# Kernel optimization log

Hardware: AMD Instinct MI355X
Metric: run time of the kernel (lower is better)

The kernel has to match this reference:

```python
import jax, jax.numpy as jnp
import numpy as np

B, S, L, F, CD, NH, E, HID = 4, 1024, 256, 512, 768, 8, 8, 2048


def _xavier(k, shape):
    std = float(np.sqrt(1.0 / (shape[-2] + shape[-1])))
    return jax.random.normal(k, shape, dtype=jnp.float32) * std


def setup_inputs() -> dict:
    key = jax.random.key(0)
    ks = iter(jax.random.split(key, 64))
    nk = lambda: next(ks)
    inp = {}
    inp['x_r'] = jax.random.normal(nk(), (B, S, F), jnp.float32)
    inp['x_i'] = jax.random.normal(nk(), (B, S, F), jnp.float32)
    inp['ctx_r'] = jax.random.normal(nk(), (B, L, CD), jnp.float32)
    inp['ctx_i'] = jax.random.normal(nk(), (B, L, CD), jnp.float32)
    inp['ln1_g'] = jnp.ones((F,), jnp.float32)
    inp['ln2_g'] = jnp.ones((F,), jnp.float32)
    inp['ln3_g'] = jnp.ones((F,), jnp.float32)
    for pref, shp in [('sa_q', (F, F)), ('sa_k', (F, F)), ('sa_v', (F, F)), ('sa_o', (F, F)),
                      ('ca_q', (F, F)), ('ca_k', (CD, F)), ('ca_v', (CD, F)), ('ca_o', (F, F))]:
        inp[pref + 'Wr'] = _xavier(nk(), shp)
        inp[pref + 'Wi'] = _xavier(nk(), shp)
        inp[pref + 'br'] = jnp.zeros((F,), jnp.float32)
        inp[pref + 'bi'] = jnp.zeros((F,), jnp.float32)
    inp['moe_W1r'] = _xavier(nk(), (E, F, HID))
    inp['moe_W1i'] = _xavier(nk(), (E, F, HID))
    inp['moe_b1r'] = jnp.zeros((E, HID), jnp.float32)
    inp['moe_b1i'] = jnp.zeros((E, HID), jnp.float32)
    inp['moe_mb'] = jnp.zeros((E, HID), jnp.float32)  # modReLU bias
    inp['moe_W2r'] = _xavier(nk(), (E, HID, F))
    inp['moe_W2i'] = _xavier(nk(), (E, HID, F))
    inp['moe_b2r'] = jnp.zeros((E, F), jnp.float32)
    inp['moe_b2i'] = jnp.zeros((E, F), jnp.float32)
    return inp


def _clin(xr, xi, Wr, Wi, br, bi):
    # (xr + i xi) @ (Wr + i Wi) + (br + i bi)
    return xr @ Wr - xi @ Wi + br, xr @ Wi + xi @ Wr + bi


def _cln(xr, xi, g, eps=1e-6):
    amp = jnp.sqrt(xr * xr + xi * xi + eps)
    s = g * (amp / (jnp.mean(amp, axis=-1, keepdims=True) + eps)) / (amp + eps)
    return xr * s, xi * s


def _modrelu(xr, xi, b, eps=1e-10):
    amp = jnp.sqrt(xr * xr + xi * xi + eps)
    s = jax.nn.relu(amp + b) / (amp + eps)
    return xr * s, xi * s


def _cattn(xr, xi, cr, ci, qWr, qWi, qbr, qbi, kWr, kWi, kbr, kbi,
           vWr, vWi, vbr, vbi, oWr, oWi, obr, obi, nh):
    qr, qi = _clin(xr, xi, qWr, qWi, qbr, qbi)
    kr, ki = _clin(cr, ci, kWr, kWi, kbr, kbi)
    vr, vi = _clin(cr, ci, vWr, vWi, vbr, vbi)
    Bt, Sq, Ft = qr.shape
    Sk = kr.shape[1]
    d = Ft // nh
    sp = lambda t: t.reshape(Bt, t.shape[1], nh, d).transpose(0, 2, 1, 3)  # b n s d
    Qr, Qi, Kr, Ki, Vr, Vi = sp(qr), sp(qi), sp(kr), sp(ki), sp(vr), sp(vi)
    scale = 1.0 / float(d) ** 0.5
    scores = (jnp.einsum('bnqd,bnkd->bnqk', Qr, Kr)
              + jnp.einsum('bnqd,bnkd->bnqk', Qi, Ki)) * scale
    w = jax.nn.softmax(scores, axis=-1)
    mix = lambda t: jnp.einsum('bnqk,bnkd->bnqd', w, t).transpose(0, 2, 1, 3).reshape(Bt, Sq, Ft)
    return _clin(mix(Vr), mix(Vi), oWr, oWi, obr, obi)


def reference(x_r, x_i, ctx_r, ctx_i, ln1_g, ln2_g, ln3_g,
              sa_qWr, sa_qWi, sa_qbr, sa_qbi, sa_kWr, sa_kWi, sa_kbr, sa_kbi,
              sa_vWr, sa_vWi, sa_vbr, sa_vbi, sa_oWr, sa_oWi, sa_obr, sa_obi,
              ca_qWr, ca_qWi, ca_qbr, ca_qbi, ca_kWr, ca_kWi, ca_kbr, ca_kbi,
              ca_vWr, ca_vWi, ca_vbr, ca_vbi, ca_oWr, ca_oWi, ca_obr, ca_obi,
              moe_W1r, moe_W1i, moe_b1r, moe_b1i, moe_mb,
              moe_W2r, moe_W2i, moe_b2r, moe_b2i):
    # self-attention block
    hr, hi = _cln(x_r, x_i, ln1_g)
    ar, ai = _cattn(hr, hi, hr, hi, sa_qWr, sa_qWi, sa_qbr, sa_qbi,
                    sa_kWr, sa_kWi, sa_kbr, sa_kbi, sa_vWr, sa_vWi, sa_vbr, sa_vbi,
                    sa_oWr, sa_oWi, sa_obr, sa_obi, NH)
    xr, xi = x_r + ar, x_i + ai
    # cross-attention block
    hr, hi = _cln(xr, xi, ln2_g)
    ar, ai = _cattn(hr, hi, ctx_r, ctx_i, ca_qWr, ca_qWi, ca_qbr, ca_qbi,
                    ca_kWr, ca_kWi, ca_kbr, ca_kbi, ca_vWr, ca_vWi, ca_vbr, ca_vbi,
                    ca_oWr, ca_oWi, ca_obr, ca_obi, NH)
    xr, xi = xr + ar, xi + ai
    # phase-routed MoE block
    hr, hi = _cln(xr, xi, ln3_g)
    phase = jnp.arctan2(hi, hr)
    token_phase = jnp.arctan2(jnp.mean(jnp.sin(phase), axis=-1),
                              jnp.mean(jnp.cos(phase), axis=-1))
    idx = jnp.clip(jnp.floor((token_phase + jnp.pi) / (2.0 * jnp.pi) * E).astype(jnp.int32), 0, E - 1)
    acc_r = jnp.zeros_like(hr)
    acc_i = jnp.zeros_like(hi)
    for e in range(E):  # dense-compute-then-mask, faithful to source
        ur, ui = _clin(hr, hi, moe_W1r[e], moe_W1i[e], moe_b1r[e], moe_b1i[e])
        ur, ui = _modrelu(ur, ui, moe_mb[e])
        yr, yi = _clin(ur, ui, moe_W2r[e], moe_W2i[e], moe_b2r[e], moe_b2i[e])
        m = (idx == e).astype(hr.dtype)[..., None]
        acc_r = acc_r + yr * m
        acc_i = acc_i + yi * m
    xr, xi = xr + acc_r, xi + acc_i
    return jnp.stack([xr, xi])  # [2, B, S, F] real/imag
```

## Files before the change

kernel.cpp:

```cpp
#include <hip/hip_runtime.h>
#include <hip/hip_bf16.h>
#include <math.h>


#define NTOK 4096
#define FF   512
#define CDIM 768
#define NEXP 8
#define HID  2048
#define TMAX 72
#define NPAD (TMAX * 64)

typedef __hip_bfloat16 bf16;
typedef short bf16x8 __attribute__((ext_vector_type(8)));
typedef float f32x4  __attribute__((ext_vector_type(4)));

__device__ __forceinline__ short f2bf(float x) {
    unsigned u = __float_as_uint(x);
    unsigned r = (u + 0x7fff + ((u >> 16) & 1)) >> 16;
    return (short)r;
}
__device__ __forceinline__ float bf2f(short s) {
    return __uint_as_float(((unsigned)(unsigned short)s) << 16);
}

__global__ __launch_bounds__(256)
void cln_kernel(const float* __restrict__ xr, const float* __restrict__ xi,
                const float* __restrict__ g,
                float* __restrict__ hr, float* __restrict__ hi)
{
    const int F = FF;
    long base = (long)blockIdx.x * F;
    int t = threadIdx.x;
    int j0 = t, j1 = t + 256;
    float xr0 = xr[base + j0], xi0 = xi[base + j0];
    float xr1 = xr[base + j1], xi1 = xi[base + j1];
    float a0 = sqrtf(xr0 * xr0 + xi0 * xi0 + 1e-6f);
    float a1 = sqrtf(xr1 * xr1 + xi1 * xi1 + 1e-6f);
    float s = a0 + a1;
#pragma unroll
    for (int off = 32; off >= 1; off >>= 1) s += __shfl_xor(s, off);
    __shared__ float wsum[4];
    if ((t & 63) == 0) wsum[t >> 6] = s;
    __syncthreads();
    float mean = (wsum[0] + wsum[1] + wsum[2] + wsum[3]) * (1.0f / 512.0f);
    float d0 = g[j0] * (a0 / (mean + 1e-6f)) / (a0 + 1e-6f);
    float d1 = g[j1] * (a1 / (mean + 1e-6f)) / (a1 + 1e-6f);
    hr[base + j0] = xr0 * d0;  hi[base + j0] = xi0 * d0;
    hr[base + j1] = xr1 * d1;  hi[base + j1] = xi1 * d1;
}

__global__ __launch_bounds__(256)
void expandA_x3(const float* __restrict__ sR, const float* __restrict__ sI,
                bf16* __restrict__ dR, bf16* __restrict__ dI, int K)
{
    int k = blockIdx.x * 256 + threadIdx.x;
    int m = blockIdx.y;
    long s = (long)m * K + k;
    long d = (long)m * 3 * K + k;
    float a = sR[s];
    bf16 ah = __float2bfloat16(a);
    bf16 al = __float2bfloat16(a - __bfloat162float(ah));
    dR[d] = ah; dR[d + K] = al; dR[d + 2 * K] = ah;
    float b = sI[s];
    bf16 bh = __float2bfloat16(b);
    bf16 bl = __float2bfloat16(b - __bfloat162float(bh));
    dI[d] = bh; dI[d + K] = bl; dI[d + 2 * K] = bh;
}

__global__ __launch_bounds__(256)
void convA_plain(const float* __restrict__ sR, const float* __restrict__ sI,
                 bf16* __restrict__ dR, bf16* __restrict__ dI, int K)
{
    int k = blockIdx.x * 256 + threadIdx.x;
    long s = (long)blockIdx.y * K + k;
    dR[s] = __float2bfloat16(sR[s]);
    dI[s] = __float2bfloat16(sI[s]);
}

__global__ __launch_bounds__(256)
void expandW_x3_packed(const float* __restrict__ sR, const float* __restrict__ sI,
                       bf16* __restrict__ dR, bf16* __restrict__ dI,
                       int N, int kdiv )
{
    int g = blockIdx.x * 256 + threadIdx.x;
    int nt = g >> 6, l = g & 63;
    int kc = blockIdx.y;
    int t3 = (kc >= kdiv) + (kc >= 2 * kdiv);
    int kb = (kc - t3 * kdiv) * 32 + (l >> 4) * 8;
    int n  = nt * 16 + (l & 15);
    long dbase = ((long)kc * (N >> 4) + nt) * 512 + l * 8;
#pragma unroll
    for (int j = 0; j < 8; j++) {
        float a = sR[(long)(kb + j) * N + n];
        bf16 ah = __float2bfloat16(a);
        dR[dbase + j] = (t3 < 2) ? ah : __float2bfloat16(a - __bfloat162float(ah));
        float b = sI[(long)(kb + j) * N + n];
        bf16 bh = __float2bfloat16(b);
        dI[dbase + j] = (t3 < 2) ? bh : __float2bfloat16(b - __bfloat162float(bh));
    }
}

__global__ __launch_bounds__(256)
void convW_packed(const float* __restrict__ sR, const float* __restrict__ sI,
                  bf16* __restrict__ dR, bf16* __restrict__ dI,
                  int N, long estride)
{
    int g = blockIdx.x * 256 + threadIdx.x;
    int nt = g >> 6, l = g & 63;
    int kc = blockIdx.y;
    int e  = blockIdx.z;
    const float* srcR = sR + (long)e * estride;
    const float* srcI = sI + (long)e * estride;
    bf16* dstR = dR + (long)e * estride;
    bf16* dstI = dI + (long)e * estride;
    int kb = kc * 32 + (l >> 4) * 8;
    int n  = nt * 16 + (l & 15);
    long dbase = ((long)kc * (N >> 4) + nt) * 512 + l * 8;
#pragma unroll
    for (int j = 0; j < 8; j++) {
        dstR[dbase + j] = __float2bfloat16(srcR[(long)(kb + j) * N + n]);
        dstI[dbase + j] = __float2bfloat16(srcI[(long)(kb + j) * N + n]);
    }
}

template<bool EXPERT, bool GATHER, bool MODRELU, bool RESID, bool OUTBF16>
__global__ __launch_bounds__(256)
void cgemm_mfma(const bf16* __restrict__ Ar, const bf16* __restrict__ Ai, int lda,
                const bf16* __restrict__ Wr, const bf16* __restrict__ Wi,
                long wstride, int ntTot,
                const float* __restrict__ br, const float* __restrict__ bi, int bstride,
                const float* __restrict__ mb,
                const float* __restrict__ Rr, const float* __restrict__ Ri,
                void* __restrict__ Crv, void* __restrict__ Civ, int ldc, int Kp,
                const int* __restrict__ order, const int* __restrict__ tileExpert)
{
    __shared__ short sA[8192];
    __shared__ short sW[8192];
    int tm = blockIdx.x, tn = blockIdx.y;
    if (EXPERT) {
        int e = tileExpert[tm];
        if (e < 0) return;
        Wr += (long)e * wstride;  Wi += (long)e * wstride;
        br += (long)e * bstride;  bi += (long)e * bstride;
        if (MODRELU) mb += (long)e * bstride;
    }
    int t = threadIdx.x;
    int m = t & 63, jj = t >> 6;
    int aldsLane = (jj << 4) + (m & 15);
    int mt = m >> 4;
    long abase; bool aok = true;
    {
        int arow = tm * 64 + m;
        if (GATHER) { int g = order[arow]; aok = (g >= 0); abase = (long)(aok ? g : 0) * lda; }
        else abase = (long)arow * lda;
    }
    int wl = t & 63, wb = t >> 6;
    int l = t & 63, w = t >> 6;
    int wm = w & 1, wn = w >> 1;

    f32x4 z = {0.f, 0.f, 0.f, 0.f};
    f32x4 accR[2][2], accI[2][2];
#pragma unroll
    for (int a = 0; a < 2; a++)
#pragma unroll
        for (int b = 0; b < 2; b++) { accR[a][b] = z; accI[a][b] = z; }

    const bf16x8 sgn = {(short)0x8000,(short)0x8000,(short)0x8000,(short)0x8000,
                        (short)0x8000,(short)0x8000,(short)0x8000,(short)0x8000};

    for (int k0 = 0; k0 < Kp; k0 += 64) {
        __syncthreads();
#pragma unroll
        for (int ri = 0; ri < 2; ri++) {
            const bf16* src = ri ? Ai : Ar;
#pragma unroll
            for (int kc = 0; kc < 2; kc++) {
                bf16x8 v = {};
                if (!GATHER || aok)
                    v = *(const bf16x8*)&src[abase + k0 + kc * 32 + jj * 8];
                *(bf16x8*)&sA[((((ri * 2 + kc) << 2) + mt) << 9) + aldsLane * 8] = v;
            }
        }
        int kc0 = k0 >> 5;
#pragma unroll
        for (int it = 0; it < 4; it++) {
            int b  = (it << 2) + wb;
            int ri = b >> 3, kc = (b >> 2) & 1, ntl = b & 3;
            const bf16* src = ri ? Wi : Wr;
            bf16x8 v = *(const bf16x8*)&src[(((long)(kc0 + kc) * ntTot + tn * 4 + ntl) << 9) + wl * 8];
            *(bf16x8*)&sW[((((ri * 2 + kc) << 2) + ntl) << 9) + wl * 8] = v;
        }
        __syncthreads();
#pragma unroll
        for (int kc = 0; kc < 2; kc++) {
            bf16x8 arf[2], aif[2], naf[2], wrf[2], wif[2];
#pragma unroll
            for (int s = 0; s < 2; s++) {
                arf[s] = *(const bf16x8*)&sA[(((kc << 2) + wm * 2 + s) << 9) + l * 8];
                aif[s] = *(const bf16x8*)&sA[((((2 + kc) << 2) + wm * 2 + s) << 9) + l * 8];
                naf[s] = aif[s] ^ sgn;
                wrf[s] = *(const bf16x8*)&sW[(((kc << 2) + wn * 2 + s) << 9) + l * 8];
                wif[s] = *(const bf16x8*)&sW[((((2 + kc) << 2) + wn * 2 + s) << 9) + l * 8];
            }
#pragma unroll
            for (int sm = 0; sm < 2; sm++)
#pragma unroll
                for (int sn = 0; sn < 2; sn++) {
                    accR[sm][sn] = __builtin_amdgcn_mfma_f32_16x16x32_bf16(arf[sm], wrf[sn], accR[sm][sn], 0, 0, 0);
                    accR[sm][sn] = __builtin_amdgcn_mfma_f32_16x16x32_bf16(naf[sm], wif[sn], accR[sm][sn], 0, 0, 0);
                    accI[sm][sn] = __builtin_amdgcn_mfma_f32_16x16x32_bf16(arf[sm], wif[sn], accI[sm][sn], 0, 0, 0);
                    accI[sm][sn] = __builtin_amdgcn_mfma_f32_16x16x32_bf16(aif[sm], wrf[sn], accI[sm][sn], 0, 0, 0);
                }
        }
    }
#pragma unroll
    for (int sm = 0; sm < 2; sm++)
#pragma unroll
        for (int sn = 0; sn < 2; sn++) {
            int row0 = tm * 64 + (wm * 2 + sm) * 16 + (l >> 4) * 4;
            int col  = tn * 64 + (wn * 2 + sn) * 16 + (l & 15);
            float bre = br[col], bie = bi[col];
            float mbe = MODRELU ? mb[col] : 0.f;
#pragma unroll
            for (int v = 0; v < 4; v++) {
                int row = row0 + v;
                float vr = accR[sm][sn][v] + bre;
                float vi = accI[sm][sn][v] + bie;
                if (MODRELU) {
                    float amp = sqrtf(vr * vr + vi * vi + 1e-10f);
                    float sc = fmaxf(amp + mbe, 0.f) / (amp + 1e-10f);
                    vr *= sc; vi *= sc;
                }
                long cidx = (long)row * ldc + col;
                if (RESID) { vr += Rr[cidx]; vi += Ri[cidx]; }
                if (OUTBF16) {
                    ((bf16*)Crv)[cidx] = __float2bfloat16(vr);
                    ((bf16*)Civ)[cidx] = __float2bfloat16(vi);
                } else {
                    ((float*)Crv)[cidx] = vr;
                    ((float*)Civ)[cidx] = vi;
                }
            }
        }
}

__global__ __launch_bounds__(256)
void cattn_mfma(const float* __restrict__ qr, const float* __restrict__ qi,
                const float* __restrict__ kr, const float* __restrict__ ki,
                const float* __restrict__ vr, const float* __restrict__ vi,
                float* __restrict__ mr, float* __restrict__ mi,
                int S, int Sk)
{
    __shared__ short sK[8192];
    __shared__ short sV[8192];
    __shared__ short sP[5120];
    const int F = FF;
    int qt = blockIdx.x, h = blockIdx.y, b = blockIdx.z;
    int t = threadIdx.x;
    int w = t >> 6, l = t & 63, q = l >> 4, n16 = l & 15;

    bf16x8 qh_[2][2], ql_[2][2];
    {
        long qbase = ((long)(b * S + qt * 64 + w * 16 + n16)) * F + h * 64 + q * 8;
#pragma unroll
        for (int ri = 0; ri < 2; ri++) {
            const float* src = ri ? qi : qr;
#pragma unroll
            for (int c = 0; c < 2; c++) {
#pragma unroll
                for (int j = 0; j < 8; j++) {
                    float x = src[qbase + c * 32 + j];
                    short xh = f2bf(x);
                    qh_[ri][c][j] = xh;
                    ql_[ri][c][j] = f2bf(x - bf2f(xh));
                }
            }
        }
    }

    f32x4 zf = {0.f, 0.f, 0.f, 0.f};
    f32x4 oR[4], oI[4];
#pragma unroll
    for (int nt = 0; nt < 4; nt++) { oR[nt] = zf; oI[nt] = zf; }
    float m_run[4] = {-3.0e38f, -3.0e38f, -3.0e38f, -3.0e38f};
    float l_run[4] = {0.f, 0.f, 0.f, 0.f};

    int nkt = Sk >> 5;
    for (int kt = 0; kt < nkt; kt++) {
        __syncthreads();
#pragma unroll
        for (int it = 0; it < 2; it++) {
            int s = t + 256 * it;
            int sl = s & 63, g = s >> 6;
            int ri = g >> 2, c = (g >> 1) & 1, nt = g & 1;
            int sq = sl >> 4, sn = sl & 15;
            const float* src = ri ? ki : kr;
            long base = ((long)(b * Sk + kt * 32 + nt * 16 + sn)) * F + h * 64 + c * 32 + sq * 8;
            int outH = ((((ri * 2 + 0) * 2 + c) * 2 + nt) * 64 + sl) * 8;
            int outL = ((((ri * 2 + 1) * 2 + c) * 2 + nt) * 64 + sl) * 8;
#pragma unroll
            for (int j = 0; j < 8; j++) {
                float x = src[base + j];
                short xh = f2bf(x);
                sK[outH + j] = xh;
                sK[outL + j] = f2bf(x - bf2f(xh));
            }
        }
#pragma unroll
        for (int it = 0; it < 2; it++) {
            int s = t + 256 * it;
            int sl = s & 63, g = s >> 6;
            int ri = g >> 2, nt = g & 3;
            int sq = sl >> 4, sn = sl & 15;
            const float* src = ri ? vi : vr;
            long base = ((long)(b * Sk + kt * 32 + sq * 8)) * F + h * 64 + nt * 16 + sn;
            int outH = (((ri * 2 + 0) * 4 + nt) * 64 + sl) * 8;
            int outL = (((ri * 2 + 1) * 4 + nt) * 64 + sl) * 8;
#pragma unroll
            for (int j = 0; j < 8; j++) {
                float x = src[base + (long)j * F];
                short xh = f2bf(x);
                sV[outH + j] = xh;
                sV[outL + j] = f2bf(x - bf2f(xh));
            }
        }
        __syncthreads();

        f32x4 sc[2];
        sc[0] = zf; sc[1] = zf;
#pragma unroll
        for (int nt = 0; nt < 2; nt++) {
#pragma unroll
            for (int ri = 0; ri < 2; ri++) {
                bf16x8 kh0 = *(const bf16x8*)&sK[((((ri * 2 + 0) * 2 + 0) * 2 + nt) * 64 + l) * 8];
                bf16x8 kh1 = *(const bf16x8*)&sK[((((ri * 2 + 0) * 2 + 1) * 2 + nt) * 64 + l) * 8];
                bf16x8 kl0 = *(const bf16x8*)&sK[((((ri * 2 + 1) * 2 + 0) * 2 + nt) * 64 + l) * 8];
                bf16x8 kl1 = *(const bf16x8*)&sK[((((ri * 2 + 1) * 2 + 1) * 2 + nt) * 64 + l) * 8];
                sc[nt] = __builtin_amdgcn_mfma_f32_16x16x32_bf16(qh_[ri][0], kh0, sc[nt], 0, 0, 0);
                sc[nt] = __builtin_amdgcn_mfma_f32_16x16x32_bf16(qh_[ri][1], kh1, sc[nt], 0, 0, 0);
                sc[nt] = __builtin_amdgcn_mfma_f32_16x16x32_bf16(ql_[ri][0], kh0, sc[nt], 0, 0, 0);
                sc[nt] = __builtin_amdgcn_mfma_f32_16x16x32_bf16(ql_[ri][1], kh1, sc[nt], 0, 0, 0);
                sc[nt] = __builtin_amdgcn_mfma_f32_16x16x32_bf16(qh_[ri][0], kl0, sc[nt], 0, 0, 0);
                sc[nt] = __builtin_amdgcn_mfma_f32_16x16x32_bf16(qh_[ri][1], kl1, sc[nt], 0, 0, 0);
            }
        }
        float alpha[4];
#pragma unroll
        for (int v = 0; v < 4; v++) {
            float s0 = sc[0][v] * 0.125f, s1 = sc[1][v] * 0.125f;
            float mx = fmaxf(s0, s1);
            mx = fmaxf(mx, __shfl_xor(mx, 1));
            mx = fmaxf(mx, __shfl_xor(mx, 2));
            mx = fmaxf(mx, __shfl_xor(mx, 4));
            mx = fmaxf(mx, __shfl_xor(mx, 8));
            float mnew = fmaxf(m_run[v], mx);
            float p0 = expf(s0 - mnew), p1 = expf(s1 - mnew);
            sc[0][v] = p0; sc[1][v] = p1;
            float ps = p0 + p1;
            ps += __shfl_xor(ps, 1);
            ps += __shfl_xor(ps, 2);
            ps += __shfl_xor(ps, 4);
            ps += __shfl_xor(ps, 8);
            alpha[v] = expf(m_run[v] - mnew);
            l_run[v] = l_run[v] * alpha[v] + ps;
            m_run[v] = mnew;
        }
#pragma unroll
        for (int nt = 0; nt < 4; nt++)
#pragma unroll
            for (int v = 0; v < 4; v++) { oR[nt][v] *= alpha[v]; oI[nt][v] *= alpha[v]; }
        int pbase = w * 1280;
#pragma unroll
        for (int nt = 0; nt < 2; nt++)
#pragma unroll
            for (int v = 0; v < 4; v++) {
                float p = sc[nt][v];
                short ph = f2bf(p);
                short pl = f2bf(p - bf2f(ph));
                int idx = pbase + (q * 4 + v) * 40 + nt * 16 + n16;
                sP[idx] = ph;
                sP[idx + 640] = pl;
            }
        bf16x8 pH = *(const bf16x8*)&sP[pbase + n16 * 40 + q * 8];
        bf16x8 pL = *(const bf16x8*)&sP[pbase + 640 + n16 * 40 + q * 8];
#pragma unroll
        for (int nt = 0; nt < 4; nt++) {
            bf16x8 vh = *(const bf16x8*)&sV[(((0 * 2 + 0) * 4 + nt) * 64 + l) * 8];
            bf16x8 vl = *(const bf16x8*)&sV[(((0 * 2 + 1) * 4 + nt) * 64 + l) * 8];
            oR[nt] = __builtin_amdgcn_mfma_f32_16x16x32_bf16(pH, vh, oR[nt], 0, 0, 0);
            oR[nt] = __builtin_amdgcn_mfma_f32_16x16x32_bf16(pL, vh, oR[nt], 0, 0, 0);
            oR[nt] = __builtin_amdgcn_mfma_f32_16x16x32_bf16(pH, vl, oR[nt], 0, 0, 0);
            bf16x8 wh = *(const bf16x8*)&sV[(((1 * 2 + 0) * 4 + nt) * 64 + l) * 8];
            bf16x8 wl2 = *(const bf16x8*)&sV[(((1 * 2 + 1) * 4 + nt) * 64 + l) * 8];
            oI[nt] = __builtin_amdgcn_mfma_f32_16x16x32_bf16(pH, wh, oI[nt], 0, 0, 0);
            oI[nt] = __builtin_amdgcn_mfma_f32_16x16x32_bf16(pL, wh, oI[nt], 0, 0, 0);
            oI[nt] = __builtin_amdgcn_mfma_f32_16x16x32_bf16(pH, wl2, oI[nt], 0, 0, 0);
        }
    }
#pragma unroll
    for (int v = 0; v < 4; v++) {
        float inv = 1.0f / l_run[v];
        long obase = ((long)(b * S + qt * 64 + w * 16 + q * 4 + v)) * F + h * 64 + n16;
#pragma unroll
        for (int nt = 0; nt < 4; nt++) {
            mr[obase + nt * 16] = oR[nt][v] * inv;
            mi[obase + nt * 16] = oI[nt][v] * inv;
        }
    }
}

__global__ __launch_bounds__(256)
void route_kernel(const float* __restrict__ hr, const float* __restrict__ hi,
                  int* __restrict__ eidx)
{
    const int F = FF;
    long base = (long)blockIdx.x * F;
// ... 87 lines not shown
extern "C" void kernel_launch(void* const* d_in, const int* in_sizes, int n_in,
                              void* d_out, int out_size, void* d_ws, size_t ws_size,
                              hipStream_t stream)
{
    (void)in_sizes; (void)n_in; (void)out_size; (void)ws_size;
    const float* x_r   = (const float*)d_in[0];
    const float* x_i   = (const float*)d_in[1];
    const float* ctx_r = (const float*)d_in[2];
    const float* ctx_i = (const float*)d_in[3];
    const float* ln1_g = (const float*)d_in[4];
    const float* ln2_g = (const float*)d_in[5];
    const float* ln3_g = (const float*)d_in[6];
    const float* sa_qWr = (const float*)d_in[7];   const float* sa_qWi = (const float*)d_in[8];
    const float* sa_qbr = (const float*)d_in[9];   const float* sa_qbi = (const float*)d_in[10];
    const float* sa_kWr = (const float*)d_in[11];  const float* sa_kWi = (const float*)d_in[12];
    const float* sa_kbr = (const float*)d_in[13];  const float* sa_kbi = (const float*)d_in[14];
    const float* sa_vWr = (const float*)d_in[15];  const float* sa_vWi = (const float*)d_in[16];
    const float* sa_vbr = (const float*)d_in[17];  const float* sa_vbi = (const float*)d_in[18];
    const float* sa_oWr = (const float*)d_in[19];  const float* sa_oWi = (const float*)d_in[20];
    const float* sa_obr = (const float*)d_in[21];  const float* sa_obi = (const float*)d_in[22];
    const float* ca_qWr = (const float*)d_in[23];  const float* ca_qWi = (const float*)d_in[24];
    const float* ca_qbr = (const float*)d_in[25];  const float* ca_qbi = (const float*)d_in[26];
    const float* ca_kWr = (const float*)d_in[27];  const float* ca_kWi = (const float*)d_in[28];
    const float* ca_kbr = (const float*)d_in[29];  const float* ca_kbi = (const float*)d_in[30];
    const float* ca_vWr = (const float*)d_in[31];  const float* ca_vWi = (const float*)d_in[32];
    const float* ca_vbr = (const float*)d_in[33];  const float* ca_vbi = (const float*)d_in[34];
    const float* ca_oWr = (const float*)d_in[35];  const float* ca_oWi = (const float*)d_in[36];
    const float* ca_obr = (const float*)d_in[37];  const float* ca_obi = (const float*)d_in[38];
    const float* moe_W1r = (const float*)d_in[39]; const float* moe_W1i = (const float*)d_in[40];
    const float* moe_b1r = (const float*)d_in[41]; const float* moe_b1i = (const float*)d_in[42];
    const float* moe_mb  = (const float*)d_in[43];
    const float* moe_W2r = (const float*)d_in[44]; const float* moe_W2i = (const float*)d_in[45];
    const float* moe_b2r = (const float*)d_in[46]; const float* moe_b2i = (const float*)d_in[47];
    float* out = (float*)d_out;

    char* W = (char*)d_ws;
    const long NF = (long)NTOK * FF;
    float* xr = (float*)(W + 0 * NF * 4);
    float* xi = (float*)(W + 1 * NF * 4);
    float* hr = (float*)(W + 2 * NF * 4);
    float* hi = (float*)(W + 3 * NF * 4);
    char* poolB = W + 4 * NF * 4;
    float* qr = (float*)poolB;                float* qi = (float*)(poolB + NF * 4);
    float* kr = (float*)(poolB + 2 * NF * 4); float* ki = (float*)(poolB + 3 * NF * 4);
    float* vr = (float*)(poolB + 4 * NF * 4); float* vi = (float*)(poolB + 5 * NF * 4);
    float* mr = (float*)(poolB + 6 * NF * 4); float* mi = (float*)(poolB + 7 * NF * 4);
    bf16* u_r = (bf16*)poolB;
    bf16* u_i = (bf16*)(poolB + 18874368);
    float* y_r = (float*)(poolB + 37748736);
    float* y_i = (float*)(poolB + 37748736 + 9437184);
    bf16* h3r = (bf16*)(poolB + 56623104);
    bf16* h3i = (bf16*)(poolB + 56623104 + 4194304);
    char* Q = W + 12 * NF * 4;
    bf16* A1r = (bf16*)Q;                   bf16* A1i = (bf16*)(Q + 12582912);
    bf16* A2r = (bf16*)(Q + 25165824);      bf16* A2i = (bf16*)(Q + 25165824 + 4718592);
    char* WQ = Q + 34603008;
    bf16* saq_r = (bf16*)(WQ + 0 * 1572864);  bf16* saq_i = (bf16*)(WQ + 1 * 1572864);
    bf16* sak_r = (bf16*)(WQ + 2 * 1572864);  bf16* sak_i = (bf16*)(WQ + 3 * 1572864);
    bf16* sav_r = (bf16*)(WQ + 4 * 1572864);  bf16* sav_i = (bf16*)(WQ + 5 * 1572864);
    bf16* sao_r = (bf16*)(WQ + 6 * 1572864);  bf16* sao_i = (bf16*)(WQ + 7 * 1572864);
    bf16* caq_r = (bf16*)(WQ + 8 * 1572864);  bf16* caq_i = (bf16*)(WQ + 9 * 1572864);
    bf16* cao_r = (bf16*)(WQ + 10 * 1572864); bf16* cao_i = (bf16*)(WQ + 11 * 1572864);
    bf16* cak_r = (bf16*)(WQ + 12 * 1572864);
    bf16* cak_i = (bf16*)(WQ + 12 * 1572864 + 2359296);
    bf16* cav_r = (bf16*)(WQ + 12 * 1572864 + 2 * 2359296);
    bf16* cav_i = (bf16*)(WQ + 12 * 1572864 + 3 * 2359296);
    bf16* Wm_r = (bf16*)Q;
    bf16* Wm_i = (bf16*)(Q + 16777216);
    int* eidx       = (int*)(W + 12 * NF * 4 + 62914560);
    int* order      = eidx + NTOK;
    int* tileExpert = order + NPAD;

    dim3 blk(256);
    const long W1S = (long)FF * HID;

    expandW_x3_packed<<<dim3(8, 48), blk, 0, stream>>>(sa_qWr, sa_qWi, saq_r, saq_i, FF, 16);
    expandW_x3_packed<<<dim3(8, 48), blk, 0, stream>>>(sa_kWr, sa_kWi, sak_r, sak_i, FF, 16);
    expandW_x3_packed<<<dim3(8, 48), blk, 0, stream>>>(sa_vWr, sa_vWi, sav_r, sav_i, FF, 16);
    expandW_x3_packed<<<dim3(8, 48), blk, 0, stream>>>(sa_oWr, sa_oWi, sao_r, sao_i, FF, 16);
    expandW_x3_packed<<<dim3(8, 48), blk, 0, stream>>>(ca_qWr, ca_qWi, caq_r, caq_i, FF, 16);
    expandW_x3_packed<<<dim3(8, 48), blk, 0, stream>>>(ca_oWr, ca_oWi, cao_r, cao_i, FF, 16);
    expandW_x3_packed<<<dim3(8, 72), blk, 0, stream>>>(ca_kWr, ca_kWi, cak_r, cak_i, FF, 24);
    expandW_x3_packed<<<dim3(8, 72), blk, 0, stream>>>(ca_vWr, ca_vWi, cav_r, cav_i, FF, 24);

    cln_kernel<<<NTOK, blk, 0, stream>>>(x_r, x_i, ln1_g, hr, hi);
    expandA_x3<<<dim3(2, NTOK), blk, 0, stream>>>(hr, hi, A1r, A1i, FF);
    cgemm_mfma<false,false,false,false,false><<<dim3(64, 8), blk, 0, stream>>>(
        A1r, A1i, 1536, saq_r, saq_i, 0, 32, sa_qbr, sa_qbi, 0, nullptr,
        nullptr, nullptr, qr, qi, FF, 1536, nullptr, nullptr);
    cgemm_mfma<false,false,false,false,false><<<dim3(64, 8), blk, 0, stream>>>(
        A1r, A1i, 1536, sak_r, sak_i, 0, 32, sa_kbr, sa_kbi, 0, nullptr,
        nullptr, nullptr, kr, ki, FF, 1536, nullptr, nullptr);
    cgemm_mfma<false,false,false,false,false><<<dim3(64, 8), blk, 0, stream>>>(
        A1r, A1i, 1536, sav_r, sav_i, 0, 32, sa_vbr, sa_vbi, 0, nullptr,
        nullptr, nullptr, vr, vi, FF, 1536, nullptr, nullptr);
    cattn_mfma<<<dim3(16, 8, 4), blk, 0, stream>>>(qr, qi, kr, ki, vr, vi,
                                                   mr, mi, 1024, 1024);
    expandA_x3<<<dim3(2, NTOK), blk, 0, stream>>>(mr, mi, A1r, A1i, FF);
    cgemm_mfma<false,false,false,true,false><<<dim3(64, 8), blk, 0, stream>>>(
        A1r, A1i, 1536, sao_r, sao_i, 0, 32, sa_obr, sa_obi, 0, nullptr,
        x_r, x_i, xr, xi, FF, 1536, nullptr, nullptr);

    cln_kernel<<<NTOK, blk, 0, stream>>>(xr, xi, ln2_g, hr, hi);
    expandA_x3<<<dim3(2, NTOK), blk, 0, stream>>>(hr, hi, A1r, A1i, FF);
    cgemm_mfma<false,false,false,false,false><<<dim3(64, 8), blk, 0, stream>>>(
        A1r, A1i, 1536, caq_r, caq_i, 0, 32, ca_qbr, ca_qbi, 0, nullptr,
        nullptr, nullptr, qr, qi, FF, 1536, nullptr, nullptr);
    expandA_x3<<<dim3(3, 1024), blk, 0, stream>>>(ctx_r, ctx_i, A2r, A2i, CDIM);
    cgemm_mfma<false,false,false,false,false><<<dim3(16, 8), blk, 0, stream>>>(
        A2r, A2i, 2304, cak_r, cak_i, 0, 32, ca_kbr, ca_kbi, 0, nullptr,
        nullptr, nullptr, kr, ki, FF, 2304, nullptr, nullptr);
    cgemm_mfma<false,false,false,false,false><<<dim3(16, 8), blk, 0, stream>>>(
        A2r, A2i, 2304, cav_r, cav_i, 0, 32, ca_vbr, ca_vbi, 0, nullptr,
        nullptr, nullptr, vr, vi, FF, 2304, nullptr, nullptr);
    cattn_mfma<<<dim3(16, 8, 4), blk, 0, stream>>>(qr, qi, kr, ki, vr, vi,
                                                   mr, mi, 1024, 256);
    expandA_x3<<<dim3(2, NTOK), blk, 0, stream>>>(mr, mi, A1r, A1i, FF);
    cgemm_mfma<false,false,false,true,false><<<dim3(64, 8), blk, 0, stream>>>(
        A1r, A1i, 1536, cao_r, cao_i, 0, 32, ca_obr, ca_obi, 0, nullptr,
        xr, xi, xr, xi, FF, 1536, nullptr, nullptr);

    cln_kernel<<<NTOK, blk, 0, stream>>>(xr, xi, ln3_g, hr, hi);
    route_kernel<<<NTOK, blk, 0, stream>>>(hr, hi, eidx);
    moe_build_kernel<<<1, blk, 0, stream>>>(eidx, order, tileExpert);
    convA_plain<<<dim3(2, NTOK), blk, 0, stream>>>(hr, hi, h3r, h3i, FF);
    convW_packed<<<dim3(32, 16, 8), blk, 0, stream>>>(moe_W1r, moe_W1i, Wm_r, Wm_i, HID, W1S);
    cgemm_mfma<true,true,true,false,true><<<dim3(TMAX, 32), blk, 0, stream>>>(
        h3r, h3i, FF, Wm_r, Wm_i, W1S, 128, moe_b1r, moe_b1i, HID, moe_mb,
        nullptr, nullptr, u_r, u_i, HID, FF, order, tileExpert);
    convW_packed<<<dim3(8, 64, 8), blk, 0, stream>>>(moe_W2r, moe_W2i, Wm_r, Wm_i, FF, W1S);
    cgemm_mfma<true,false,false,false,false><<<dim3(TMAX, 8), blk, 0, stream>>>(
        u_r, u_i, HID, Wm_r, Wm_i, W1S, 32, moe_b2r, moe_b2i, FF, nullptr,
        nullptr, nullptr, y_r, y_i, FF, HID, order, tileExpert);
    combine_kernel<<<NPAD, blk, 0, stream>>>(order, xr, xi, y_r, y_i, out);
}
```

Measured before the change: 1.031 ms.

## Use async global-to-LDS loads, x2 split storage, batched QKV GEMMs, prepacked KV

The expanded bf16 split operands are now stored as only hi/lo (x2) instead of hi/lo/hi, and the GEMM remaps its K index on the fly so the third term reuses the hi part. This cuts expansion traffic and buffer size. GEMM tile loads use global_load_lds direct-to-LDS copies, and Q/K/V (plus cross-attn K/V) projections are batched into one launch via a z grid dimension. K/V are pre-split into packed bf16 hi/lo tiles by a separate kernel so attention can bulk-copy them, and expf becomes __expf. This adds a pack kernel, reuses buffers for the packed data, and the fast exp slightly changes numerics.

Result: faster. 894.5 us (-13.2%).

```diff
diff --git a/kernel.cpp b/kernel.cpp
--- a/kernel.cpp
+++ b/kernel.cpp
@@ -15,6 +15,8 @@
 typedef short bf16x8 __attribute__((ext_vector_type(8)));
 typedef float f32x4  __attribute__((ext_vector_type(4)));
 
+struct Ptr6 { const float* p[6]; };
+
 __device__ __forceinline__ short f2bf(float x) {
     unsigned u = __float_as_uint(x);
     unsigned r = (u + 0x7fff + ((u >> 16) & 1)) >> 16;
@@ -22,6 +24,11 @@
 }
 __device__ __forceinline__ float bf2f(short s) {
     return __uint_as_float(((unsigned)(unsigned short)s) << 16);
+}
+__device__ __forceinline__ void gload16(const void* g, void* l) {
+    __builtin_amdgcn_global_load_lds(
+        (const __attribute__((address_space(1))) unsigned int*)g,
+        (__attribute__((address_space(3))) unsigned int*)l, 16, 0, 0);
 }
 
 __global__ __launch_bounds__(256)
@@ -51,21 +58,19 @@
 }
 
 __global__ __launch_bounds__(256)
-void expandA_x3(const float* __restrict__ sR, const float* __restrict__ sI,
+void expandA_x2(const float* __restrict__ sR, const float* __restrict__ sI,
                 bf16* __restrict__ dR, bf16* __restrict__ dI, int K)
 {
     int k = blockIdx.x * 256 + threadIdx.x;
     int m = blockIdx.y;
     long s = (long)m * K + k;
-    long d = (long)m * 3 * K + k;
+    long d = (long)m * 2 * K + k;
     float a = sR[s];
     bf16 ah = __float2bfloat16(a);
-    bf16 al = __float2bfloat16(a - __bfloat162float(ah));
-    dR[d] = ah; dR[d + K] = al; dR[d + 2 * K] = ah;
+    dR[d] = ah; dR[d + K] = __float2bfloat16(a - __bfloat162float(ah));
     float b = sI[s];
     bf16 bh = __float2bfloat16(b);
-    bf16 bl = __float2bfloat16(b - __bfloat162float(bh));
-    dI[d] = bh; dI[d + K] = bl; dI[d + 2 * K] = bh;
+    dI[d] = bh; dI[d + K] = __float2bfloat16(b - __bfloat162float(bh));
 }
 
 __global__ __launch_bounds__(256)
@@ -79,25 +84,25 @@
 }
 
 __global__ __launch_bounds__(256)
-void expandW_x3_packed(const float* __restrict__ sR, const float* __restrict__ sI,
+void expandW_x2_packed(const float* __restrict__ sR, const float* __restrict__ sI,
                        bf16* __restrict__ dR, bf16* __restrict__ dI,
-                       int N, int kdiv )
+                       int N, int kdiv)
 {
     int g = blockIdx.x * 256 + threadIdx.x;
     int nt = g >> 6, l = g & 63;
     int kc = blockIdx.y;
-    int t3 = (kc >= kdiv) + (kc >= 2 * kdiv);
-    int kb = (kc - t3 * kdiv) * 32 + (l >> 4) * 8;
+    int lo = (kc >= kdiv);
+    int kb = (kc - (lo ? kdiv : 0)) * 32 + (l >> 4) * 8;
     int n  = nt * 16 + (l & 15);
     long dbase = ((long)kc * (N >> 4) + nt) * 512 + l * 8;
 #pragma unroll
     for (int j = 0; j < 8; j++) {
         float a = sR[(long)(kb + j) * N + n];
         bf16 ah = __float2bfloat16(a);
-        dR[dbase + j] = (t3 < 2) ? ah : __float2bfloat16(a - __bfloat162float(ah));
+        dR[dbase + j] = lo ? __float2bfloat16(a - __bfloat162float(ah)) : ah;
         float b = sI[(long)(kb + j) * N + n];
         bf16 bh = __float2bfloat16(b);
-        dI[dbase + j] = (t3 < 2) ? bh : __float2bfloat16(b - __bfloat162float(bh));
+        dI[dbase + j] = lo ? __float2bfloat16(b - __bfloat162float(bh)) : bh;
     }
 }
 
@@ -124,73 +129,75 @@
     }
 }
 
-template<bool EXPERT, bool GATHER, bool MODRELU, bool RESID, bool OUTBF16>
-__global__ __launch_bounds__(256)
-void cgemm_mfma(const bf16* __restrict__ Ar, const bf16* __restrict__ Ai, int lda,
-                const bf16* __restrict__ Wr, const bf16* __restrict__ Wi,
-                long wstride, int ntTot,
-                const float* __restrict__ br, const float* __restrict__ bi, int bstride,
-                const float* __restrict__ mb,
+template<bool X3, bool EXPERT, bool GATHER, bool MODRELU, bool RESID, bool OUTBF16>
+__global__ __launch_bounds__(256)
+void cgemm_mfma(const bf16* __restrict__ Ar, const bf16* __restrict__ Ai,
+                int lda, int Kreal,
+                const bf16* __restrict__ Wr0, const bf16* __restrict__ Wi0,
+                long wz, long westride, int ntTot, int kdiv,
+                Ptr6 bias, int bstride, const float* __restrict__ mb,
                 const float* __restrict__ Rr, const float* __restrict__ Ri,
-                void* __restrict__ Crv, void* __restrict__ Civ, int ldc, int Kp,
+                void* __restrict__ Cr0, void* __restrict__ Ci0, long cz,
+                int ldc, int Kp,
                 const int* __restrict__ order, const int* __restrict__ tileExpert)
 {
     __shared__ short sA[8192];
     __shared__ short sW[8192];
-    int tm = blockIdx.x, tn = blockIdx.y;
+    int tm = blockIdx.x, tn = blockIdx.y, z = blockIdx.z;
+    const bf16* Wr = Wr0 + (long)z * wz;
+    const bf16* Wi = Wi0 + (long)z * wz;
+    const float* br = bias.p[2 * z];
+    const float* bi = bias.p[2 * z + 1];
+    void* Crv = (char*)Cr0 + (long)z * cz;
+    void* Civ = (char*)Ci0 + (long)z * cz;
     if (EXPERT) {
         int e = tileExpert[tm];
         if (e < 0) return;
-        Wr += (long)e * wstride;  Wi += (long)e * wstride;
-        br += (long)e * bstride;  bi += (long)e * bstride;
+        Wr += (long)e * westride;  Wi += (long)e * westride;
+        br += (long)e * bstride;   bi += (long)e * bstride;
         if (MODRELU) mb += (long)e * bstride;
     }
     int t = threadIdx.x;
-    int m = t & 63, jj = t >> 6;
-    int aldsLane = (jj << 4) + (m & 15);
-    int mt = m >> 4;
-    long abase; bool aok = true;
-    {
-        int arow = tm * 64 + m;
-        if (GATHER) { int g = order[arow]; aok = (g >= 0); abase = (long)(aok ? g : 0) * lda; }
-        else abase = (long)arow * lda;
-    }
-    int wl = t & 63, wb = t >> 6;
-    int l = t & 63, w = t >> 6;
-    int wm = w & 1, wn = w >> 1;
-
-    f32x4 z = {0.f, 0.f, 0.f, 0.f};
+    int l = t & 63, jj = t >> 6;
+    int riS = jj >> 1, kcS = jj & 1;
+    const bf16* Asrc = riS ? Ai : Ar;
+    const bf16* Wsrc = riS ? Wi : Wr;
+    int kq8 = (l >> 4) * 8;
+    long arb[4];
+#pragma unroll
+    for (int mt = 0; mt < 4; mt++) {
+        int grow = tm * 64 + mt * 16 + (l & 15);
+        int tok = grow;
+        if (GATHER) { int gg = order[grow]; tok = (gg < 0) ? 0 : gg; }
+        arb[mt] = (long)tok * lda;
+    }
+    int wm = jj & 1, wn = jj >> 1;
+
+    f32x4 zf = {0.f, 0.f, 0.f, 0.f};
     f32x4 accR[2][2], accI[2][2];
 #pragma unroll
     for (int a = 0; a < 2; a++)
 #pragma unroll
-        for (int b = 0; b < 2; b++) { accR[a][b] = z; accI[a][b] = z; }
+        for (int b = 0; b < 2; b++) { accR[a][b] = zf; accI[a][b] = zf; }
 
     const bf16x8 sgn = {(short)0x8000,(short)0x8000,(short)0x8000,(short)0x8000,
                         (short)0x8000,(short)0x8000,(short)0x8000,(short)0x8000};
 
     for (int k0 = 0; k0 < Kp; k0 += 64) {
         __syncthreads();
-#pragma unroll
-        for (int ri = 0; ri < 2; ri++) {
-            const bf16* src = ri ? Ai : Ar;
-#pragma unroll
-            for (int kc = 0; kc < 2; kc++) {
-                bf16x8 v = {};
-                if (!GATHER || aok)
-                    v = *(const bf16x8*)&src[abase + k0 + kc * 32 + jj * 8];
-                *(bf16x8*)&sA[((((ri * 2 + kc) << 2) + mt) << 9) + aldsLane * 8] = v;
-            }
-        }
-        int kc0 = k0 >> 5;
-#pragma unroll
-        for (int it = 0; it < 4; it++) {
-            int b  = (it << 2) + wb;
-            int ri = b >> 3, kc = (b >> 2) & 1, ntl = b & 3;
-            const bf16* src = ri ? Wi : Wr;
-            bf16x8 v = *(const bf16x8*)&src[(((long)(kc0 + kc) * ntTot + tn * 4 + ntl) << 9) + wl * 8];
-            *(bf16x8*)&sW[((((ri * 2 + kc) << 2) + ntl) << 9) + wl * 8] = v;
-        }
+        int lc = k0 + kcS * 32;
+        int acol = (X3 && lc >= 2 * Kreal) ? lc - 2 * Kreal : lc;
+#pragma unroll
+        for (int mt = 0; mt < 4; mt++)
+            gload16(Asrc + arb[mt] + acol + kq8,
+                    &sA[(((riS * 2 + kcS) << 2) + mt) << 9]);
+        int kcl = (k0 >> 5) + kcS;
+        int pkc = (X3 && kcl >= kdiv) ? kcl - kdiv : kcl;
+        const bf16* wbase = Wsrc + (((long)pkc * ntTot + tn * 4) << 9) + l * 8;
+#pragma unroll
+        for (int ntl = 0; ntl < 4; ntl++)
+            gload16(wbase + (ntl << 9),
+                    &sW[(((riS * 2 + kcS) << 2) + ntl) << 9]);
         __syncthreads();
 #pragma unroll
         for (int kc = 0; kc < 2; kc++) {
@@ -246,9 +253,56 @@
 }
 
 __global__ __launch_bounds__(256)
+void pack_kv(const float* __restrict__ kr, const float* __restrict__ ki,
+             const float* __restrict__ vr, const float* __restrict__ vi,
+             short* __restrict__ pK, short* __restrict__ pV, int Sk)
+{
+    const int F = FF;
+    int kt = blockIdx.x, h = blockIdx.y, b = blockIdx.z;
+    int nkt = gridDim.x;
+    long blkbase = ((long)((b * 8 + h) * nkt) + kt) * 8192;
+    int t = threadIdx.x;
+#pragma unroll
+    for (int it = 0; it < 2; it++) {
+        int s = t + 256 * it;
+        int sl = s & 63, g = s >> 6;
+        int ri = g >> 2, c = (g >> 1) & 1, nt = g & 1;
+        int sq = sl >> 4, sn = sl & 15;
+        const float* src = ri ? ki : kr;
+        long base = ((long)(b * Sk + kt * 32 + nt * 16 + sn)) * F + h * 64 + c * 32 + sq * 8;
+        long outH = blkbase + ((((ri * 2 + 0) * 2 + c) * 2 + nt) * 64 + sl) * 8;
+        long outL = blkbase + ((((ri * 2 + 1) * 2 + c) * 2 + nt) * 64 + sl) * 8;
+#pragma unroll
+        for (int j = 0; j < 8; j++) {
+            float x = src[base + j];
+            short xh = f2bf(x);
+            pK[outH + j] = xh;
+            pK[outL + j] = f2bf(x - bf2f(xh));
+        }
+    }
+#pragma unroll
+    for (int it = 0; it < 2; it++) {
+        int s = t + 256 * it;
+        int sl = s & 63, g = s >> 6;
+        int ri = g >> 2, nt = g & 3;
+        int sq = sl >> 4, sn = sl & 15;
+        const float* src = ri ? vi : vr;
+        long base = ((long)(b * Sk + kt * 32 + sq * 8)) * F + h * 64 + nt * 16 + sn;
+        long outH = blkbase + (((ri * 2 + 0) * 4 + nt) * 64 + sl) * 8;
+        long outL = blkbase + (((ri * 2 + 1) * 4 + nt) * 64 + sl) * 8;
+#pragma unroll
+        for (int j = 0; j < 8; j++) {
+            float x = src[base + (long)j * F];
+            short xh = f2bf(x);
+            pV[outH + j] = xh;
+            pV[outL + j] = f2bf(x - bf2f(xh));
+        }
+    }
+}
+
+__global__ __launch_bounds__(256)
 void cattn_mfma(const float* __restrict__ qr, const float* __restrict__ qi,
-                const float* __restrict__ kr, const float* __restrict__ ki,
-                const float* __restrict__ vr, const float* __restrict__ vi,
+                const short* __restrict__ pK, const short* __restrict__ pV,
                 float* __restrict__ mr, float* __restrict__ mi,
                 int S, int Sk)
 {
@@ -268,12 +322,14 @@
             const float* src = ri ? qi : qr;
 #pragma unroll
             for (int c = 0; c < 2; c++) {
+                float vv[8];
+                *(float4*)&vv[0] = *(const float4*)&src[qbase + c * 32];
+                *(float4*)&vv[4] = *(const float4*)&src[qbase + c * 32 + 4];
 #pragma unroll
                 for (int j = 0; j < 8; j++) {
-                    float x = src[qbase + c * 32 + j];
-                    short xh = f2bf(x);
+                    short xh = f2bf(vv[j]);
                     qh_[ri][c][j] = xh;
-                    ql_[ri][c][j] = f2bf(x - bf2f(xh));
+                    ql_[ri][c][j] = f2bf(vv[j] - bf2f(xh));
                 }
             }
         }
@@ -287,43 +343,15 @@
     float l_run[4] = {0.f, 0.f, 0.f, 0.f};
 
     int nkt = Sk >> 5;
+    long pbh = (long)((b * 8 + h) * nkt) * 8192;
     for (int kt = 0; kt < nkt; kt++) {
         __syncthreads();
-#pragma unroll
-        for (int it = 0; it < 2; it++) {
-            int s = t + 256 * it;
-            int sl = s & 63, g = s >> 6;
-            int ri = g >> 2, c = (g >> 1) & 1, nt = g & 1;
-            int sq = sl >> 4, sn = sl & 15;
-            const float* src = ri ? ki : kr;
-            long base = ((long)(b * Sk + kt * 32 + nt * 16 + sn)) * F + h * 64 + c * 32 + sq * 8;
-            int outH = ((((ri * 2 + 0) * 2 + c) * 2 + nt) * 64 + sl) * 8;
-            int outL = ((((ri * 2 + 1) * 2 + c) * 2 + nt) * 64 + sl) * 8;
-#pragma unroll
-            for (int j = 0; j < 8; j++) {
-                float x = src[base + j];
-                short xh = f2bf(x);
-                sK[outH + j] = xh;
-                sK[outL + j] = f2bf(x - bf2f(xh));
-            }
-        }
-#pragma unroll
-        for (int it = 0; it < 2; it++) {
-            int s = t + 256 * it;
-            int sl = s & 63, g = s >> 6;
-            int ri = g >> 2, nt = g & 3;
-            int sq = sl >> 4, sn = sl & 15;
-            const float* src = ri ? vi : vr;
-            long base = ((long)(b * Sk + kt * 32 + sq * 8)) * F + h * 64 + nt * 16 + sn;
-            int outH = (((ri * 2 + 0) * 4 + nt) * 64 + sl) * 8;
-            int outL = (((ri * 2 + 1) * 4 + nt) * 64 + sl) * 8;
-#pragma unroll
-            for (int j = 0; j < 8; j++) {
-                float x = src[base + (long)j * F];
-                short xh = f2bf(x);
-                sV[outH + j] = xh;
-                sV[outL + j] = f2bf(x - bf2f(xh));
-            }
+        long pb = pbh + (long)kt * 8192;
+#pragma unroll
+        for (int i = 0; i < 4; i++) {
+            int bk = w * 4 + i;
+            gload16(pK + pb + (bk << 9) + l * 8, &sK[bk << 9]);
+            gload16(pV + pb + (bk << 9) + l * 8, &sV[bk << 9]);
         }
         __syncthreads();
 
@@ -355,14 +383,14 @@
             mx = fmaxf(mx, __shfl_xor(mx, 4));
             mx = fmaxf(mx, __shfl_xor(mx, 8));
             float mnew = fmaxf(m_run[v], mx);
-            float p0 = expf(s0 - mnew), p1 = expf(s1 - mnew);
+            float p0 = __expf(s0 - mnew), p1 = __expf(s1 - mnew);
             sc[0][v] = p0; sc[1][v] = p1;
             float ps = p0 + p1;
             ps += __shfl_xor(ps, 1);
             ps += __shfl_xor(ps, 2);
             ps += __shfl_xor(ps, 4);
             ps += __shfl_xor(ps, 8);
-            alpha[v] = expf(m_run[v] - mnew);
+            alpha[v] = __expf(m_run[v] - mnew);
             l_run[v] = l_run[v] * alpha[v] + ps;
             m_run[v] = mnew;
         }
@@ -556,19 +584,23 @@
     bf16* h3r = (bf16*)(poolB + 56623104);
     bf16* h3i = (bf16*)(poolB + 56623104 + 4194304);
     char* Q = W + 12 * NF * 4;
-    bf16* A1r = (bf16*)Q;                   bf16* A1i = (bf16*)(Q + 12582912);
-    bf16* A2r = (bf16*)(Q + 25165824);      bf16* A2i = (bf16*)(Q + 25165824 + 4718592);
-    char* WQ = Q + 34603008;
-    bf16* saq_r = (bf16*)(WQ + 0 * 1572864);  bf16* saq_i = (bf16*)(WQ + 1 * 1572864);
-    bf16* sak_r = (bf16*)(WQ + 2 * 1572864);  bf16* sak_i = (bf16*)(WQ + 3 * 1572864);
-    bf16* sav_r = (bf16*)(WQ + 4 * 1572864);  bf16* sav_i = (bf16*)(WQ + 5 * 1572864);
-    bf16* sao_r = (bf16*)(WQ + 6 * 1572864);  bf16* sao_i = (bf16*)(WQ + 7 * 1572864);
-    bf16* caq_r = (bf16*)(WQ + 8 * 1572864);  bf16* caq_i = (bf16*)(WQ + 9 * 1572864);
-    bf16* cao_r = (bf16*)(WQ + 10 * 1572864); bf16* cao_i = (bf16*)(WQ + 11 * 1572864);
-    bf16* cak_r = (bf16*)(WQ + 12 * 1572864);
-    bf16* cak_i = (bf16*)(WQ + 12 * 1572864 + 2359296);
-    bf16* cav_r = (bf16*)(WQ + 12 * 1572864 + 2 * 2359296);
-    bf16* cav_i = (bf16*)(WQ + 12 * 1572864 + 3 * 2359296);
+    bf16* A1r = (bf16*)Q;
+    bf16* A1i = (bf16*)(Q + 8388608);
+    bf16* A2r = (bf16*)(Q + 16777216);
+    bf16* A2i = (bf16*)(Q + 19922944);
+    char* WQ = Q + 23068672;
+    const long PS1 = 524288;
+    const long PS2 = 786432;
+    bf16* saq_r = (bf16*)(WQ);                   bf16* saq_i = saq_r + PS1;
+    bf16* sak_r = saq_r + 2 * PS1;               bf16* sak_i = saq_r + 3 * PS1;
+    bf16* sav_r = saq_r + 4 * PS1;               bf16* sav_i = saq_r + 5 * PS1;
+    bf16* sao_r = saq_r + 6 * PS1;               bf16* sao_i = saq_r + 7 * PS1;
+    bf16* caq_r = saq_r + 8 * PS1;               bf16* caq_i = saq_r + 9 * PS1;
+    bf16* cao_r = saq_r + 10 * PS1;              bf16* cao_i = saq_r + 11 * PS1;
+    bf16* cak_r = saq_r + 12 * PS1;              bf16* cak_i = cak_r + PS2;
+    bf16* cav_r = cak_r + 2 * PS2;               bf16* cav_i = cak_r + 3 * PS2;
+    short* pKbuf = (short*)hr;
+    short* pVbuf = (short*)Q;
     bf16* Wm_r = (bf16*)Q;
     bf16* Wm_i = (bf16*)(Q + 16777216);
     int* eidx       = (int*)(W + 12 * NF * 4 + 62914560);
@@ -577,64 +609,63 @@
 
     dim3 blk(256);
     const long W1S = (long)FF * HID;
-
-    expandW_x3_packed<<<dim3(8, 48), blk, 0, stream>>>(sa_qWr, sa_qWi, saq_r, saq_i, FF, 16);
-    expandW_x3_packed<<<dim3(8, 48), blk, 0, stream>>>(sa_kWr, sa_kWi, sak_r, sak_i, FF, 16);
-    expandW_x3_packed<<<dim3(8, 48), blk, 0, stream>>>(sa_vWr, sa_vWi, sav_r, sav_i, FF, 16);
-    expandW_x3_packed<<<dim3(8, 48), blk, 0, stream>>>(sa_oWr, sa_oWi, sao_r, sao_i, FF, 16);
-    expandW_x3_packed<<<dim3(8, 48), blk, 0, stream>>>(ca_qWr, ca_qWi, caq_r, caq_i, FF, 16);
-    expandW_x3_packed<<<dim3(8, 48), blk, 0, stream>>>(ca_oWr, ca_oWi, cao_r, cao_i, FF, 16);
-    expandW_x3_packed<<<dim3(8, 72), blk, 0, stream>>>(ca_kWr, ca_kWi, cak_r, cak_i, FF, 24);
-    expandW_x3_packed<<<dim3(8, 72), blk, 0, stream>>>(ca_vWr, ca_vWi, cav_r, cav_i, FF, 24);
+    const long CZ = 2 * NF * 4;
+    Ptr6 bQKV = {{sa_qbr, sa_qbi, sa_kbr, sa_kbi, sa_vbr, sa_vbi}};
+    Ptr6 bSAO = {{sa_obr, sa_obi, 0, 0, 0, 0}};
+    Ptr6 bCAQ = {{ca_qbr, ca_qbi, 0, 0, 0, 0}};
+    Ptr6 bCKV = {{ca_kbr, ca_kbi, ca_vbr, ca_vbi, 0, 0}};
+    Ptr6 bCAO = {{ca_obr, ca_obi, 0, 0, 0, 0}};
+    Ptr6 bM1  = {{moe_b1r, moe_b1i, 0, 0, 0, 0}};
+    Ptr6 bM2  = {{moe_b2r, moe_b2i, 0, 0, 0, 0}};
+
+    expandW_x2_packed<<<dim3(8, 32), blk, 0, stream>>>(sa_qWr, sa_qWi, saq_r, saq_i, FF, 16);
+    expandW_x2_packed<<<dim3(8, 32), blk, 0, stream>>>(sa_kWr, sa_kWi, sak_r, sak_i, FF, 16);
+    expandW_x2_packed<<<dim3(8, 32), blk, 0, stream>>>(sa_vWr, sa_vWi, sav_r, sav_i, FF, 16);
+    expandW_x2_packed<<<dim3(8, 32), blk, 0, stream>>>(sa_oWr, sa_oWi, sao_r, sao_i, FF, 16);
+    expandW_x2_packed<<<dim3(8, 32), blk, 0, stream>>>(ca_qWr, ca_qWi, caq_r, caq_i, FF, 16);
+    expandW_x2_packed<<<dim3(8, 32), blk, 0, stream>>>(ca_oWr, ca_oWi, cao_r, cao_i, FF, 16);
+    expandW_x2_packed<<<dim3(8, 48), blk, 0, stream>>>(ca_kWr, ca_kWi, cak_r, cak_i, FF, 24);
+    expandW_x2_packed<<<dim3(8, 48), blk, 0, stream>>>(ca_vWr, ca_vWi, cav_r, cav_i, FF, 24);
 
     cln_kernel<<<NTOK, blk, 0, stream>>>(x_r, x_i, ln1_g, hr, hi);
-    expandA_x3<<<dim3(2, NTOK), blk, 0, stream>>>(hr, hi, A1r, A1i, FF);
-    cgemm_mfma<false,false,false,false,false><<<dim3(64, 8), blk, 0, stream>>>(
-        A1r, A1i, 1536, saq_r, saq_i, 0, 32, sa_qbr, sa_qbi, 0, nullptr,
-        nullptr, nullptr, qr, qi, FF, 1536, nullptr, nullptr);
-    cgemm_mfma<false,false,false,false,false><<<dim3(64, 8), blk, 0, stream>>>(
-        A1r, A1i, 1536, sak_r, sak_i, 0, 32, sa_kbr, sa_kbi, 0, nullptr,
-        nullptr, nullptr, kr, ki, FF, 1536, nullptr, nullptr);
-    cgemm_mfma<false,false,false,false,false><<<dim3(64, 8), blk, 0, stream>>>(
-        A1r, A1i, 1536, sav_r, sav_i, 0, 32, sa_vbr, sa_vbi, 0, nullptr,
-        nullptr, nullptr, vr, vi, FF, 1536, nullptr, nullptr);
-    cattn_mfma<<<dim3(16, 8, 4), blk, 0, stream>>>(qr, qi, kr, ki, vr, vi,
-                                                   mr, mi, 1024, 1024);
-    expandA_x3<<<dim3(2, NTOK), blk, 0, stream>>>(mr, mi, A1r, A1i, FF);
-    cgemm_mfma<false,false,false,true,false><<<dim3(64, 8), blk, 0, stream>>>(
-        A1r, A1i, 1536, sao_r, sao_i, 0, 32, sa_obr, sa_obi, 0, nullptr,
-        x_r, x_i, xr, xi, FF, 1536, nullptr, nullptr);
+    expandA_x2<<<dim3(2, NTOK), blk, 0, stream>>>(hr, hi, A1r, A1i, FF);
+    cgemm_mfma<true,false,false,false,false,false><<<dim3(64, 8, 3), blk, 0, stream>>>(
+        A1r, A1i, 1024, 512, saq_r, saq_i, 2 * PS1, 0, 32, 16,
+        bQKV, 0, nullptr, nullptr, nullptr, qr, qi, CZ, FF, 1536, nullptr, nullptr);
+    pack_kv<<<dim3(32, 8, 4), blk, 0, stream>>>(kr, ki, vr, vi, pKbuf, pVbuf, 1024);
+    cattn_mfma<<<dim3(16, 8, 4), blk, 0, stream>>>(qr, qi, pKbuf, pVbuf, mr, mi, 1024, 1024);
+    expandA_x2<<<dim3(2, NTOK), blk, 0, stream>>>(mr, mi, A1r, A1i, FF);
+    cgemm_mfma<true,false,false,false,true,false><<<dim3(64, 8, 1), blk, 0, stream>>>(
+        A1r, A1i, 1024, 512, sao_r, sao_i, 0, 0, 32, 16,
+        bSAO, 0, nullptr, x_r, x_i, xr, xi, 0, FF, 1536, nullptr, nullptr);
 
     cln_kernel<<<NTOK, blk, 0, stream>>>(xr, xi, ln2_g, hr, hi);
-    expandA_x3<<<dim3(2, NTOK), blk, 0, stream>>>(hr, hi, A1r, A1i, FF);
-    cgemm_mfma<false,false,false,false,false><<<dim3(64, 8), blk, 0, stream>>>(
-        A1r, A1i, 1536, caq_r, caq_i, 0, 32, ca_qbr, ca_qbi, 0, nullptr,
-        nullptr, nullptr, qr, qi, FF, 1536, nullptr, nullptr);
-    expandA_x3<<<dim3(3, 1024), blk, 0, stream>>>(ctx_r, ctx_i, A2r, A2i, CDIM);
-    cgemm_mfma<false,false,false,false,false><<<dim3(16, 8), blk, 0, stream>>>(
-        A2r, A2i, 2304, cak_r, cak_i, 0, 32, ca_kbr, ca_kbi, 0, nullptr,
-        nullptr, nullptr, kr, ki, FF, 2304, nullptr, nullptr);
-    cgemm_mfma<false,false,false,false,false><<<dim3(16, 8), blk, 0, stream>>>(
-        A2r, A2i, 2304, cav_r, cav_i, 0, 32, ca_vbr, ca_vbi, 0, nullptr,
-        nullptr, nullptr, vr, vi, FF, 2304, nullptr, nullptr);
-    cattn_mfma<<<dim3(16, 8, 4), blk, 0, stream>>>(qr, qi, kr, ki, vr, vi,
-                                                   mr, mi, 1024, 256);
-    expandA_x3<<<dim3(2, NTOK), blk, 0, stream>>>(mr, mi, A1r, A1i, FF);
-    cgemm_mfma<false,false,false,true,false><<<dim3(64, 8), blk, 0, stream>>>(
-        A1r, A1i, 1536, cao_r, cao_i, 0, 32, ca_obr, ca_obi, 0, nullptr,
-        xr, xi, xr, xi, FF, 1536, nullptr, nullptr);
+    expandA_x2<<<dim3(2, NTOK), blk, 0, stream>>>(hr, hi, A1r, A1i, FF);
+    cgemm_mfma<true,false,false,false,false,false><<<dim3(64, 8, 1), blk, 0, stream>>>(
+        A1r, A1i, 1024, 512, caq_r, caq_i, 0, 0, 32, 16,
+        bCAQ, 0, nullptr, nullptr, nullptr, qr, qi, 0, FF, 1536, nullptr, nullptr);
+    expandA_x2<<<dim3(3, 1024), blk, 0, stream>>>(ctx_r, ctx_i, A2r, A2i, CDIM);
+    cgemm_mfma<true,false,false,false,false,false><<<dim3(16, 8, 2), blk, 0, stream>>>(
+        A2r, A2i, 1536, 768, cak_r, cak_i, 2 * PS2, 0, 32, 24,
+        bCKV, 0, nullptr, nullptr, nullptr, kr, ki, CZ, FF, 2304, nullptr, nullptr);
+    pack_kv<<<dim3(8, 8, 4), blk, 0, stream>>>(kr, ki, vr, vi, pKbuf, pVbuf, 256);
+    cattn_mfma<<<dim3(16, 8, 4), blk, 0, stream>>>(qr, qi, pKbuf, pVbuf, mr, mi, 1024, 256);
+    expandA_x2<<<dim3(2, NTOK), blk, 0, stream>>>(mr, mi, A1r, A1i, FF);
+    cgemm_mfma<true,false,false,false,true,false><<<dim3(64, 8, 1), blk, 0, stream>>>(
+        A1r, A1i, 1024, 512, cao_r, cao_i, 0, 0, 32, 16,
+        bCAO, 0, nullptr, xr, xi, xr, xi, 0, FF, 1536, nullptr, nullptr);
 
     cln_kernel<<<NTOK, blk, 0, stream>>>(xr, xi, ln3_g, hr, hi);
     route_kernel<<<NTOK, blk, 0, stream>>>(hr, hi, eidx);
     moe_build_kernel<<<1, blk, 0, stream>>>(eidx, order, tileExpert);
     convA_plain<<<dim3(2, NTOK), blk, 0, stream>>>(hr, hi, h3r, h3i, FF);
     convW_packed<<<dim3(32, 16, 8), blk, 0, stream>>>(moe_W1r, moe_W1i, Wm_r, Wm_i, HID, W1S);
-    cgemm_mfma<true,true,true,false,true><<<dim3(TMAX, 32), blk, 0, stream>>>(
-        h3r, h3i, FF, Wm_r, Wm_i, W1S, 128, moe_b1r, moe_b1i, HID, moe_mb,
-        nullptr, nullptr, u_r, u_i, HID, FF, order, tileExpert);
+    cgemm_mfma<false,true,true,true,false,true><<<dim3(TMAX, 32, 1), blk, 0, stream>>>(
+        h3r, h3i, 512, 512, Wm_r, Wm_i, 0, W1S, 128, 0,
+        bM1, HID, moe_mb, nullptr, nullptr, u_r, u_i, 0, HID, 512, order, tileExpert);
     convW_packed<<<dim3(8, 64, 8), blk, 0, stream>>>(moe_W2r, moe_W2i, Wm_r, Wm_i, FF, W1S);
-    cgemm_mfma<true,false,false,false,false><<<dim3(TMAX, 8), blk, 0, stream>>>(
-        u_r, u_i, HID, Wm_r, Wm_i, W1S, 32, moe_b2r, moe_b2i, FF, nullptr,
-        nullptr, nullptr, y_r, y_i, FF, HID, order, tileExpert);
+    cgemm_mfma<false,true,false,false,false,false><<<dim3(TMAX, 8, 1), blk, 0, stream>>>(
+        u_r, u_i, 2048, 2048, Wm_r, Wm_i, 0, W1S, 32, 0,
+        bM2, FF, nullptr, nullptr, nullptr, y_r, y_i, 0, FF, 2048, nullptr, tileExpert);
     combine_kernel<<<NPAD, blk, 0, stream>>>(order, xr, xi, y_r, y_i, out);
 }
```
